# Kernel tuning notes

Hardware: AMD Instinct MI355X
Metric: run time of the kernel (lower is better)

Reference implementation:

```python
import jax, jax.numpy as jnp
import numpy as np

N_NODES = 100000
N_EDGES = 1600000
DIM = 128


def setup_inputs() -> dict:
    key = jax.random.key(0)
    ks = jax.random.split(key, 8)
    s = 1.0 / np.sqrt(DIM)
    return {
        "x": jax.random.normal(ks[0], (N_NODES, DIM), dtype=jnp.float32),
        "edge_index": jax.random.randint(ks[1], (2, N_EDGES), 0, N_NODES, dtype=jnp.int64),
        "W1_l": jax.random.normal(ks[2], (DIM, DIM), dtype=jnp.float32) * s,
        "b1": jnp.zeros((DIM,), dtype=jnp.float32),
        "W1_r": jax.random.normal(ks[3], (DIM, DIM), dtype=jnp.float32) * s,
        "W2_l": jax.random.normal(ks[4], (DIM, DIM), dtype=jnp.float32) * s,
        "b2": jnp.zeros((DIM,), dtype=jnp.float32),
        "W2_r": jax.random.normal(ks[5], (DIM, DIM), dtype=jnp.float32) * s,
    }


def _sage_conv(h, src, dst, n, W_l, b, W_r):
    # mean aggregation of source-node features onto target nodes
    agg = jax.ops.segment_sum(h[src], dst, num_segments=n)          # [N, D]
    deg = jax.ops.segment_sum(jnp.ones_like(src, dtype=h.dtype), dst, num_segments=n)
    agg = agg / jnp.maximum(deg, 1.0)[:, None]
    # PyG SAGEConv: lin_l(aggr) + bias + lin_r(x)  (root weight, no bias on lin_r)
    return agg @ W_l + b + h @ W_r


def reference(x, edge_index, W1_l, b1, W1_r, W2_l, b2, W2_r):
    src, dst = edge_index[0], edge_index[1]
    n = x.shape[0]
    h = jax.nn.relu(_sage_conv(x, src, dst, n, W1_l, b1, W1_r))
    return _sage_conv(h, src, dst, n, W2_l, b2, W2_r)
```

## Files before the change

### kernel.cpp

```cpp
#include <hip/hip_runtime.h>

typedef unsigned short ushort_t;
typedef unsigned int uint_t;

typedef short bf16x8 __attribute__((ext_vector_type(8)));
typedef float f32x4 __attribute__((ext_vector_type(4)));

#define DIM 128
#define BSHIFT 8
#define BNODES 256

__device__ __forceinline__ ushort_t f2bf(float f) {
    uint_t x;
    __builtin_memcpy(&x, &f, 4);
    uint_t r = (x + 0x7fffu + ((x >> 16) & 1u)) >> 16;
    return (ushort_t)r;
}


__global__ __launch_bounds__(256) void k_prep_bhist(
        const float* __restrict__ x, ushort_t* __restrict__ xb, int n4,
        const float* __restrict__ W1l, const float* __restrict__ W1r,
        const float* __restrict__ W2l, const float* __restrict__ W2r,
        ushort_t* __restrict__ fragbuf,
        const int* __restrict__ dst, int E, int NB, int* __restrict__ bucketCount,
        int prepBlocks) {
    if ((int)blockIdx.x >= prepBlocks) {
        __shared__ int hist[512];
        int blk = blockIdx.x - prepBlocks;
        int t = threadIdx.x;
        for (int b = t; b < NB; b += 256) hist[b] = 0;
        __syncthreads();
        int per = (E + 255) / 256;
        int beg = blk * per, end = min(beg + per, E);
        for (int i = beg + t; i < end; i += 256)
            atomicAdd(&hist[dst[i] >> BSHIFT], 1);
        __syncthreads();
        for (int b = t; b < NB; b += 256) {
            int v = hist[b];
            if (v) atomicAdd(&bucketCount[b], v);
        }
        return;
    }
    int i = blockIdx.x * 256 + threadIdx.x;
    if (i < n4) {
        float4 f = ((const float4*)x)[i];
        ushort4 u;
        u.x = f2bf(f.x); u.y = f2bf(f.y); u.z = f2bf(f.z); u.w = f2bf(f.w);
        ((ushort4*)xb)[i] = u;
    } else {
        int j = i - n4;
        if (j < 2 * 64 * 64) {
            int layer = j >> 12;
            int rr = j & 4095;
            int f = rr >> 6, l = rr & 63;
            int nt = f >> 3, ks2 = f & 7;
            int col = l & 15, quad = l >> 4;
            int n = nt * 16 + col;
            int kb = ks2 * 32 + quad * 8;
            const float* Wl = layer ? W2l : W1l;
            const float* Wr = layer ? W2r : W1r;
            ushort_t* d = fragbuf + layer * 32768 + f * 512 + l * 8;
#pragma unroll
            for (int jj = 0; jj < 8; jj++) {
                int k2 = kb + jj;
                float v = (k2 < 128) ? Wl[k2 * DIM + n] : Wr[(k2 - 128) * DIM + n];
                d[jj] = f2bf(v);
            }
        }
    }
}


__global__ __launch_bounds__(256) void k_bucketize(const int* __restrict__ src,
                                                   const int* __restrict__ dst, int E, int NB,
                                                   const int* __restrict__ bucketCount,
                                                   int* __restrict__ bucketBase_out,
                                                   int* __restrict__ row_ptr, int N,
                                                   int* __restrict__ zcur,
                                                   uint_t* __restrict__ bebuf) {
    __shared__ int bbase[512];
    __shared__ int hist[512];
    __shared__ int rbase[512];
    int t = threadIdx.x;
    int i0 = t, i1 = t + 256;
    int v0 = (i0 < NB) ? bucketCount[i0] : 0;
    int v1 = (i1 < NB) ? bucketCount[i1] : 0;
    bbase[i0] = v0; bbase[i1] = v1;
    __syncthreads();
    for (int off = 1; off < 512; off <<= 1) {
        int u0 = (i0 >= off) ? bbase[i0 - off] : 0;
        int u1 = (i1 >= off) ? bbase[i1 - off] : 0;
        __syncthreads();
        bbase[i0] += u0; bbase[i1] += u1;
        __syncthreads();
    }
    bbase[i0] -= v0;
    bbase[i1] -= v1;
    if (blockIdx.x == 0) {
        if (i0 < NB) bucketBase_out[i0] = bbase[i0];
        if (i1 < NB) bucketBase_out[i1] = bbase[i1];
        if (t == 0) row_ptr[N] = E;
    }
    hist[i0] = 0; hist[i1] = 0;
    __syncthreads();
    int per = (E + gridDim.x - 1) / gridDim.x;
    int beg = blockIdx.x * per, end = min(beg + per, E);
    for (int i = beg + t; i < end; i += 256)
        atomicAdd(&hist[dst[i] >> BSHIFT], 1);
    __syncthreads();
    {
        int v = hist[i0];
        rbase[i0] = v ? (bbase[i0] + atomicAdd(&zcur[i0], v)) : 0;
        hist[i0] = 0;
        v = hist[i1];
        rbase[i1] = v ? (bbase[i1] + atomicAdd(&zcur[i1], v)) : 0;
        hist[i1] = 0;
    }
    __syncthreads();
    for (int i = beg + t; i < end; i += 256) {
        int d = dst[i], s = src[i];
        int b = d >> BSHIFT;
        int off = atomicAdd(&hist[b], 1);
        bebuf[rbase[b] + off] = ((uint_t)(d & (BNODES - 1)) << 24) | (uint_t)s;
    }
}

__global__ __launch_bounds__(256) void k_bcsr(const uint_t* __restrict__ bebuf,
                                              const int* __restrict__ bucketBase,
                                              const int* __restrict__ bucketCount, int N,
                                              int* __restrict__ row_ptr, int* __restrict__ csr) {
    __shared__ int hist[BNODES];
    __shared__ int cur[BNODES];
    int t = threadIdx.x;
    int b = blockIdx.x;
    int ebase = bucketBase[b], cnt = bucketCount[b];
    int nodeBase = b << BSHIFT;
    hist[t] = 0;
    __syncthreads();
    for (int i = t; i < cnt; i += 256)
        atomicAdd(&hist[bebuf[ebase + i] >> 24], 1);
    __syncthreads();
    int v = hist[t];
    int node = nodeBase + t;
    for (int off = 1; off < 256; off <<= 1) {
        int u = (t >= off) ? hist[t - off] : 0;
        __syncthreads();
        hist[t] += u;
        __syncthreads();
    }
    int excl = hist[t] - v;
    if (node < N) row_ptr[node] = ebase + excl;
    cur[t] = excl;
    __syncthreads();
    for (int i = t; i < cnt; i += 256) {
        uint_t e = bebuf[ebase + i];
        int dl = (int)(e >> 24);
        int pos = atomicAdd(&cur[dl], 1);
        csr[ebase + pos] = (int)(e & 0xFFFFFFu);
    }
}


__device__ __forceinline__ void acc8(float* a, uint4 p) {
    union { uint_t u; float f; } c;
    c.u = p.x << 16;         a[0] += c.f;
    c.u = p.x & 0xffff0000u; a[1] += c.f;
    c.u = p.y << 16;         a[2] += c.f;
    c.u = p.y & 0xffff0000u; a[3] += c.f;
    c.u = p.z << 16;         a[4] += c.f;
    c.u = p.z & 0xffff0000u; a[5] += c.f;
    c.u = p.w << 16;         a[6] += c.f;
    c.u = p.w & 0xffff0000u; a[7] += c.f;
}

template <bool RELU, bool OUT_BF16>
__global__ __launch_bounds__(256) void k_fused(const ushort_t* __restrict__ X,
                                               const int* __restrict__ row_ptr,
                                               const int* __restrict__ csr,
                                               const ushort_t* __restrict__ fragbuf,
                                               const float* __restrict__ bias,
                                               void* __restrict__ Out, int N) {
    __shared__ __align__(16) ushort_t tile[16 * 256];
    int t = threadIdx.x;
    int gl = t >> 4;
    int sl = t & 15;
    int node = blockIdx.x * 16 + gl;
    bool act = (node < N);
    int beg = 0, end = 0;
    if (act) {
        beg = row_ptr[node];
        end = row_ptr[node + 1];
    }

    float a[8] = {0.f, 0.f, 0.f, 0.f, 0.f, 0.f, 0.f, 0.f};
    int e = beg;
    for (; e + 4 <= end; e += 4) {
        int s0 = csr[e + 0], s1 = csr[e + 1], s2 = csr[e + 2], s3 = csr[e + 3];
        uint4 p0 = *(const uint4*)(X + (size_t)s0 * DIM + sl * 8);
        uint4 p1 = *(const uint4*)(X + (size_t)s1 * DIM + sl * 8);
        uint4 p2 = *(const uint4*)(X + (size_t)s2 * DIM + sl * 8);
        uint4 p3 = *(const uint4*)(X + (size_t)s3 * DIM + sl * 8);
        acc8(a, p0); acc8(a, p1); acc8(a, p2); acc8(a, p3);
    }
    for (; e < end; e++) {
        int s = csr[e];
        uint4 p = *(const uint4*)(X + (size_t)s * DIM + sl * 8);
        acc8(a, p);
    }
    int cnt = end - beg;
    float scl = (cnt > 0) ? 1.f / (float)cnt : 0.f;

    int swz = gl & 7;
    uint4 o;
    o.x = (uint_t)f2bf(a[0] * scl) | ((uint_t)f2bf(a[1] * scl) << 16);
    o.y = (uint_t)f2bf(a[2] * scl) | ((uint_t)f2bf(a[3] * scl) << 16);
    o.z = (uint_t)f2bf(a[4] * scl) | ((uint_t)f2bf(a[5] * scl) << 16);
    o.w = (uint_t)f2bf(a[6] * scl) | ((uint_t)f2bf(a[7] * scl) << 16);
    *(uint4*)(tile + gl * 256 + ((sl ^ swz) * 8)) = o;
    uint4 p;
    if (act) p = *(const uint4*)(X + (size_t)node * DIM + sl * 8);
    else     p = (uint4){0u, 0u, 0u, 0u};
    *(uint4*)(tile + gl * 256 + (((16 + sl) ^ swz) * 8)) = p;
    __syncthreads();

    int lane = t & 63, w = t >> 6;
    int m = lane & 15, quad = lane >> 4;
    bf16x8 af[8];
#pragma unroll
    for (int ks2 = 0; ks2 < 8; ks2++) {
        int c = (ks2 * 4 + quad) ^ (m & 7);
        af[ks2] = *(const bf16x8*)(tile + m * 256 + c * 8);
    }
    f32x4 acc0 = (f32x4){0.f, 0.f, 0.f, 0.f};
    f32x4 acc1 = (f32x4){0.f, 0.f, 0.f, 0.f};
    const ushort_t* fb0 = fragbuf + (size_t)((w * 2 + 0) * 8) * 512 + lane * 8;
    const ushort_t* fb1 = fragbuf + (size_t)((w * 2 + 1) * 8) * 512 + lane * 8;
#pragma unroll
    for (int ks2 = 0; ks2 < 8; ks2++) {
        bf16x8 b0 = *(const bf16x8*)(fb0 + ks2 * 512);
        acc0 = __builtin_amdgcn_mfma_f32_16x16x32_bf16(af[ks2], b0, acc0, 0, 0, 0);
    }
#pragma unroll
    for (int ks2 = 0; ks2 < 8; ks2++) {
        bf16x8 b1 = *(const bf16x8*)(fb1 + ks2 * 512);
        acc1 = __builtin_amdgcn_mfma_f32_16x16x32_bf16(af[ks2], b1, acc1, 0, 0, 0);
    }
    int c0 = (w * 2 + 0) * 16 + m;
    int c1 = (w * 2 + 1) * 16 + m;
    float bv0 = bias[c0], bv1 = bias[c1];

    if (OUT_BF16) {
        float r0v[4], r1v[4];
#pragma unroll
        for (int r = 0; r < 4; r++) {
            float v0 = acc0[r] + bv0, v1 = acc1[r] + bv1;
            if (RELU) { v0 = fmaxf(v0, 0.f); v1 = fmaxf(v1, 0.f); }
            r0v[r] = v0; r1v[r] = v1;
        }
        __syncthreads();
        ushort_t* to = tile;
#pragma unroll
        for (int r = 0; r < 4; r++) {
            int mrow = quad * 4 + r;
            to[mrow * 128 + c0] = f2bf(r0v[r]);
            to[mrow * 128 + c1] = f2bf(r1v[r]);
        }
        __syncthreads();
        int gl2 = t >> 4, sl2 = t & 15;
        int n2 = blockIdx.x * 16 + gl2;
        if (n2 < N) {
            uint4 vv = *(const uint4*)(to + gl2 * 128 + sl2 * 8);
            *(uint4*)((ushort_t*)Out + (size_t)n2 * DIM + sl2 * 8) = vv;
        }
    } else {
#pragma unroll
        for (int r = 0; r < 4; r++) {
            int mrow = quad * 4 + r;
            int nodeW = blockIdx.x * 16 + mrow;
            if (nodeW < N) {
                float v0 = acc0[r] + bv0;
                float v1 = acc1[r] + bv1;
                if (RELU) { v0 = fmaxf(v0, 0.f); v1 = fmaxf(v1, 0.f); }
                ((float*)Out)[(size_t)nodeW * DIM + c0] = v0;
                ((float*)Out)[(size_t)nodeW * DIM + c1] = v1;
            }
        }
    }
}


extern "C" void kernel_launch(void* const* d_in, const int* in_sizes, int n_in,
                              void* d_out, int out_size, void* d_ws, size_t ws_size,
                              hipStream_t stream) {
    const int N = in_sizes[0] / DIM;
    const int E = in_sizes[1] / 2;
    const int NB = (N + BNODES - 1) >> BSHIFT;

    const float* x   = (const float*)d_in[0];
    const int*   ei  = (const int*)d_in[1];
    const int*   src = ei;
    const int*   dst = ei + E;
    const float* W1l = (const float*)d_in[2];
    const float* b1  = (const float*)d_in[3];
    const float* W1r = (const float*)d_in[4];
    const float* W2l = (const float*)d_in[5];
    const float* b2  = (const float*)d_in[6];
    const float* W2r = (const float*)d_in[7];
    float* out = (float*)d_out;

    char* ws = (char*)d_ws;
    size_t off = 0;
    auto alloc = [&](size_t bytes) -> char* {
        char* p = ws + off;
        off = (off + bytes + 255) & ~(size_t)255;
        return p;
    };

    int*      bucketCount  = (int*)alloc((size_t)NB * 4);
    int*      zcur         = (int*)alloc((size_t)NB * 4);
    size_t    zspan        = (size_t)((char*)zcur + NB * 4 - (char*)bucketCount);
    int*      bucketBase   = (int*)alloc((size_t)NB * 4);
    int*      row_ptr      = (int*)alloc((size_t)(N + 1) * 4);
    int*      csr          = (int*)alloc((size_t)E * 4);
    uint_t*   bebuf        = (uint_t*)alloc((size_t)E * 4);
    ushort_t* xb           = (ushort_t*)alloc((size_t)N * DIM * 2);
    ushort_t* hb           = (ushort_t*)alloc((size_t)N * DIM * 2);
    ushort_t* fragbuf      = (ushort_t*)alloc((size_t)2 * 32768 * 2);

    hipMemsetAsync(bucketCount, 0, zspan, stream);

    {
        int n4 = N * DIM / 4;
        int total = n4 + 2 * 64 * 64;
        int prepBlocks = (total + 255) / 256;
        k_prep_bhist<<<dim3(prepBlocks + 256), dim3(256), 0, stream>>>(
            x, xb, n4, W1l, W1r, W2l, W2r, fragbuf,
            dst, E, NB, bucketCount, prepBlocks);
    }
    k_bucketize<<<dim3(256), dim3(256), 0, stream>>>(src, dst, E, NB, bucketCount,
                                                     bucketBase, row_ptr, N, zcur, bebuf);
    k_bcsr<<<dim3(NB), dim3(256), 0, stream>>>(bebuf, bucketBase, bucketCount, N,
                                               row_ptr, csr);

    const int ntiles = (N + 15) / 16;
    k_fused<true, true><<<dim3(ntiles), dim3(256), 0, stream>>>(
        xb, row_ptr, csr, fragbuf, b1, hb, N);
    k_fused<false, false><<<dim3(ntiles), dim3(256), 0, stream>>>(
        hb, row_ptr, csr, fragbuf + 32768, b2, out, N);

    (void)n_in; (void)out_size; (void)ws_size;
}
```

Baseline: 311.7 us.

## Sort nodes by in-degree within buckets to balance gather work per tile

New measurement: 331.0 us (median of 2 runs). 1.06x slower.

```diff
diff --git a/kernel.cpp b/kernel.cpp
--- a/kernel.cpp
+++ b/kernel.cpp
@@ -9,6 +9,7 @@
 #define DIM 128
 #define BSHIFT 8
 #define BNODES 256
+#define DBINS 64
 
 __device__ __forceinline__ ushort_t f2bf(float f) {
     uint_t x;
@@ -129,20 +130,26 @@
 __global__ __launch_bounds__(256) void k_bcsr(const uint_t* __restrict__ bebuf,
                                               const int* __restrict__ bucketBase,
                                               const int* __restrict__ bucketCount, int N,
-                                              int* __restrict__ row_ptr, int* __restrict__ csr) {
+                                              int* __restrict__ row_ptr, int* __restrict__ csr,
+                                              int* __restrict__ perm) {
     __shared__ int hist[BNODES];
     __shared__ int cur[BNODES];
+    __shared__ int dh[DBINS];
+    __shared__ int dcur2[DBINS];
     int t = threadIdx.x;
     int b = blockIdx.x;
     int ebase = bucketBase[b], cnt = bucketCount[b];
     int nodeBase = b << BSHIFT;
     hist[t] = 0;
+    if (t < DBINS) dh[t] = 0;
     __syncthreads();
     for (int i = t; i < cnt; i += 256)
         atomicAdd(&hist[bebuf[ebase + i] >> 24], 1);
     __syncthreads();
     int v = hist[t];
     int node = nodeBase + t;
+    int bin = min(v, DBINS - 1);
+    if (node < N) atomicAdd(&dh[bin], 1);
     for (int off = 1; off < 256; off <<= 1) {
         int u = (t >= off) ? hist[t - off] : 0;
         __syncthreads();
@@ -158,6 +165,20 @@
         int dl = (int)(e >> 24);
         int pos = atomicAdd(&cur[dl], 1);
         csr[ebase + pos] = (int)(e & 0xFFFFFFu);
+    }
+    if (t < DBINS) dcur2[t] = dh[t];
+    __syncthreads();
+    for (int off = 1; off < DBINS; off <<= 1) {
+        int u = (t < DBINS && t >= off) ? dcur2[t - off] : 0;
+        __syncthreads();
+        if (t < DBINS) dcur2[t] += u;
+        __syncthreads();
+    }
+    if (t < DBINS) dcur2[t] -= dh[t];
+    __syncthreads();
+    if (node < N) {
+        int pos = atomicAdd(&dcur2[bin], 1);
+        perm[nodeBase + pos] = node;
     }
 }
 
@@ -178,20 +199,24 @@
 __global__ __launch_bounds__(256) void k_fused(const ushort_t* __restrict__ X,
                                                const int* __restrict__ row_ptr,
                                                const int* __restrict__ csr,
+                                               const int* __restrict__ perm,
                                                const ushort_t* __restrict__ fragbuf,
                                                const float* __restrict__ bias,
                                                void* __restrict__ Out, int N) {
     __shared__ __align__(16) ushort_t tile[16 * 256];
+    __shared__ int nd[16];
     int t = threadIdx.x;
     int gl = t >> 4;
     int sl = t & 15;
-    int node = blockIdx.x * 16 + gl;
-    bool act = (node < N);
-    int beg = 0, end = 0;
+    int gidx = blockIdx.x * 16 + gl;
+    bool act = (gidx < N);
+    int node = 0, beg = 0, end = 0;
     if (act) {
+        node = perm[gidx];
         beg = row_ptr[node];
         end = row_ptr[node + 1];
     }
+    if (sl == 0) nd[gl] = node;
 
     float a[8] = {0.f, 0.f, 0.f, 0.f, 0.f, 0.f, 0.f, 0.f};
     int e = beg;
@@ -268,17 +293,18 @@
         }
         __syncthreads();
         int gl2 = t >> 4, sl2 = t & 15;
-        int n2 = blockIdx.x * 16 + gl2;
-        if (n2 < N) {
+        int g2 = blockIdx.x * 16 + gl2;
+        if (g2 < N) {
             uint4 vv = *(const uint4*)(to + gl2 * 128 + sl2 * 8);
-            *(uint4*)((ushort_t*)Out + (size_t)n2 * DIM + sl2 * 8) = vv;
+            *(uint4*)((ushort_t*)Out + (size_t)nd[gl2] * DIM + sl2 * 8) = vv;
         }
     } else {
 #pragma unroll
         for (int r = 0; r < 4; r++) {
             int mrow = quad * 4 + r;
-            int nodeW = blockIdx.x * 16 + mrow;
-            if (nodeW < N) {
+            int gI = blockIdx.x * 16 + mrow;
+            if (gI < N) {
+                int nodeW = nd[mrow];
                 float v0 = acc0[r] + bv0;
                 float v1 = acc1[r] + bv1;
                 if (RELU) { v0 = fmaxf(v0, 0.f); v1 = fmaxf(v1, 0.f); }
@@ -324,6 +350,7 @@
     int*      row_ptr      = (int*)alloc((size_t)(N + 1) * 4);
     int*      csr          = (int*)alloc((size_t)E * 4);
     uint_t*   bebuf        = (uint_t*)alloc((size_t)E * 4);
+    int*      perm         = (int*)alloc((size_t)N * 4);
     ushort_t* xb           = (ushort_t*)alloc((size_t)N * DIM * 2);
     ushort_t* hb           = (ushort_t*)alloc((size_t)N * DIM * 2);
     ushort_t* fragbuf      = (ushort_t*)alloc((size_t)2 * 32768 * 2);
@@ -341,13 +368,13 @@
     k_bucketize<<<dim3(256), dim3(256), 0, stream>>>(src, dst, E, NB, bucketCount,
                                                      bucketBase, row_ptr, N, zcur, bebuf);
     k_bcsr<<<dim3(NB), dim3(256), 0, stream>>>(bebuf, bucketBase, bucketCount, N,
-                                               row_ptr, csr);
+                                               row_ptr, csr, perm);
 
     const int ntiles = (N + 15) / 16;
     k_fused<true, true><<<dim3(ntiles), dim3(256), 0, stream>>>(
-        xb, row_ptr, csr, fragbuf, b1, hb, N);
+        xb, row_ptr, csr, perm, fragbuf, b1, hb, N);
     k_fused<false, false><<<dim3(ntiles), dim3(256), 0, stream>>>(
-        hb, row_ptr, csr, fragbuf + 32768, b2, out, N);
+        hb, row_ptr, csr, perm, fragbuf + 32768, b2, out, N);
 
     (void)n_in; (void)out_size; (void)ws_size;
 }
```
